# Kernel tuning notes

Hardware: AMD Instinct MI355X
Metric: run time of the kernel (lower is better)

Reference implementation:

```python
import jax, jax.numpy as jnp
import numpy as np

N_NODES, N_EDGES = 100000, 1600000
D_IN, D_H, D_OUT = 256, 128, 32


def _gcn_conv(x, W, b, row, col, norm, n):
    # GCNConv: transform, normalized gather from source nodes, scatter-sum at targets, bias.
    h = x @ W                                   # [n, d_out]
    msgs = h[row] * norm[:, None]               # [E', d_out] edge messages
    out = jax.ops.segment_sum(msgs, col, num_segments=n)
    return out + b


def setup_inputs() -> dict:
    key = jax.random.key(0)
    k = jax.random.split(key, 6)
    x = jax.random.normal(k[0], (N_NODES, D_IN), dtype=jnp.float32)
    edge_index = jax.random.randint(k[1], (2, N_EDGES), 0, N_NODES, dtype=jnp.int64)
    # Glorot-ish scaled params (GCNConv lin has no bias; bias added post-aggregation)
    W1 = jax.random.normal(k[2], (D_IN, D_H), dtype=jnp.float32) * (1.0 / np.sqrt(D_IN))
    b1 = jnp.zeros((D_H,), dtype=jnp.float32)
    W2 = jax.random.normal(k[3], (D_H, D_OUT), dtype=jnp.float32) * (1.0 / np.sqrt(D_H))
    b2 = jnp.zeros((D_OUT,), dtype=jnp.float32)
    return {"x": x, "W1": W1, "b1": b1, "W2": W2, "b2": b2, "edge_index": edge_index}


def reference(x, W1, b1, W2, b2, edge_index):
    n = x.shape[0]
    loops = jnp.arange(n, dtype=edge_index.dtype)
    row = jnp.concatenate([edge_index[0], loops])   # sources (incl. self-loops)
    col = jnp.concatenate([edge_index[1], loops])   # targets
    # symmetric normalization deg^{-1/2} (deg >= 1 because of self-loops)
    deg = jax.ops.segment_sum(jnp.ones_like(col, dtype=x.dtype), col, num_segments=n)
    dinv = deg ** -0.5
    norm = dinv[row] * dinv[col]
    h = jax.nn.relu(_gcn_conv(x, W1, b1, row, col, norm, n))
    # F.dropout(training=False) is identity in eval mode
    out = _gcn_conv(h, W2, b2, row, col, norm, n)
    return jax.nn.log_softmax(out, axis=1)
```

## Files before the change

kernel.cpp:

```cpp
#include <hip/hip_runtime.h>
#include <math.h>

#define N_NODES 100000
#define N_EDGES 1600000
#define D_IN 256
#define D_H 128
#define D_OUT 32
#define N_PAD 102400
#define NB 196
#define CAPB 10240
#define CHUNK 4096

typedef long long ll;
typedef unsigned int uint;
typedef unsigned short ushort;
typedef unsigned char uchar;
typedef short frag_ab __attribute__((ext_vector_type(8)));
typedef float frag_cd __attribute__((ext_vector_type(4)));

__device__ __forceinline__ ushort f2bf(float f) {
    uint u = __float_as_uint(f);
    u += 0x7FFFu + ((u >> 16) & 1u);
    return (ushort)(u >> 16);
}
__device__ __forceinline__ float bfl(uint u) { return __uint_as_float(u << 16); }
__device__ __forceinline__ float bfh(uint u) { return __uint_as_float(u & 0xFFFF0000u); }
__device__ __forceinline__ uint packbf(float a, float b) {
    return (uint)f2bf(a) | ((uint)f2bf(b) << 16);
}

__global__ __launch_bounds__(256) void k_prep(const float* __restrict__ W1,
                                              const float* __restrict__ W2,
                                              ushort* __restrict__ w1t,
                                              ushort* __restrict__ w2t,
                                              int* __restrict__ gcur) {
    int gi = blockIdx.x * 256 + threadIdx.x;
    if (blockIdx.x == 0) gcur[threadIdx.x] = 0;
    if (gi < D_IN * D_H) {
        int k = gi >> 7, nn = gi & 127;
        w1t[nn * D_IN + k] = f2bf(W1[gi]);
    } else if (gi < D_IN * D_H + D_H * D_OUT) {
        int j = gi - D_IN * D_H;
        int k = j >> 5, nn = j & 31;
        w2t[nn * D_H + k] = f2bf(W2[j]);
    }
}

__global__ __launch_bounds__(256, 3) void k_fused(const int* __restrict__ row,
                                                  const int* __restrict__ col,
                                                  int* __restrict__ gcur,
                                                  uint* __restrict__ pairs,
                                                  const float* __restrict__ x,
                                                  const ushort* __restrict__ w1t,
                                                  ushort* __restrict__ hxs,
                                                  int n, int e) {
    __shared__ int cnt[NB];
    __shared__ int lofs[NB];
    __shared__ int lstart[NB];
    __shared__ int sc[256];
    __shared__ uint spair[CHUNK];
    __shared__ uchar sbuck[CHUNK];
    const int t = threadIdx.x;
    const int GA = (e + CHUNK - 1) / CHUNK;
    const int bid = blockIdx.x;

    if (bid < GA) {
        if (t < NB) cnt[t] = 0;
        __syncthreads();
        const int base = bid * CHUNK;
        const int end = min(base + CHUNK, e);
        const int valid = end - base;
        int rs[16], cs[16];
#pragma unroll
        for (int j = 0; j < 16; j++) {
            int idx = base + t + j * 256;
            bool ok = idx < end;
            int c = ok ? col[idx] : 0;
            rs[j] = ok ? row[idx] : 0;
            cs[j] = ok ? c : -1;
            if (ok) atomicAdd(&cnt[c >> 9], 1);
        }
        __syncthreads();
        int v = (t < NB) ? cnt[t] : 0;
        sc[t] = v;
        __syncthreads();
        for (int o = 1; o < 256; o <<= 1) {
            int u2 = (t >= o) ? sc[t - o] : 0;
            __syncthreads();
            sc[t] += u2;
            __syncthreads();
        }
        if (t < NB) {
            lofs[t] = sc[t] - v;
            lstart[t] = (v > 0) ? atomicAdd(&gcur[t], v) : 0;
            cnt[t] = 0;
        }
        __syncthreads();
#pragma unroll
        for (int j = 0; j < 16; j++) {
            int c = cs[j];
            if (c >= 0) {
                int b = c >> 9;
                int pos = lofs[b] + atomicAdd(&cnt[b], 1);
                spair[pos] = ((uint)rs[j] << 9) | (uint)(c & 511);
                sbuck[pos] = (uchar)b;
            }
        }
        __syncthreads();
        for (int i = t; i < valid; i += 256) {
            int b = sbuck[i];
            int rel = lstart[b] + (i - lofs[b]);
            if (rel < CAPB) pairs[b * CAPB + rel] = spair[i];
        }
    } else {
        const int id = bid - GA;
        const int wv = t >> 6, lane = t & 63;
        const int lm = lane & 15, quad = lane >> 4;
        const int base = id * 128 + wv * 32;

        frag_cd acc[2][8];
#pragma unroll
        for (int mt = 0; mt < 2; mt++)
#pragma unroll
            for (int nt = 0; nt < 8; nt++) acc[mt][nt] = (frag_cd){0.f, 0.f, 0.f, 0.f};

        const float4* xr[2];
#pragma unroll
        for (int mt = 0; mt < 2; mt++) {
            int node = base + mt * 16 + lm;
            xr[mt] = (const float4*)(x + (ll)min(node, n - 1) * D_IN);
        }

#pragma unroll
        for (int ks = 0; ks < 8; ks++) {
            frag_ab a[2];
#pragma unroll
            for (int mt = 0; mt < 2; mt++) {
                float4 v0 = xr[mt][ks * 8 + quad * 2];
                float4 v1 = xr[mt][ks * 8 + quad * 2 + 1];
                uint* ap = (uint*)&a[mt];
                ap[0] = packbf(v0.x, v0.y);
                ap[1] = packbf(v0.z, v0.w);
                ap[2] = packbf(v1.x, v1.y);
                ap[3] = packbf(v1.z, v1.w);
            }
#pragma unroll
            for (int nt = 0; nt < 8; nt++) {
                frag_ab b = *(const frag_ab*)&w1t[(nt * 16 + lm) * D_IN + ks * 32 + quad * 8];
#pragma unroll
                for (int mt = 0; mt < 2; mt++)
                    acc[mt][nt] = __builtin_amdgcn_mfma_f32_16x16x32_bf16(
                        a[mt], b, acc[mt][nt], 0, 0, 0);
            }
        }

#pragma unroll
        for (int mt = 0; mt < 2; mt++) {
#pragma unroll
            for (int r = 0; r < 4; r++) {
                int node = base + mt * 16 + quad * 4 + r;
                if (node < n) {
#pragma unroll
                    for (int nt = 0; nt < 8; nt++)
                        hxs[(ll)node * D_H + nt * 16 + lm] = f2bf(acc[mt][nt][r]);
                }
            }
        }
    }
}

__global__ __launch_bounds__(512) void k_fillB(const uint* __restrict__ pairs,
                                               const int* __restrict__ gcur,
                                               int* __restrict__ deg,
                                               int* __restrict__ rp,
                                               float* __restrict__ dinv,
                                               int* __restrict__ csr_src, int n) {
    __shared__ int scsr[CAPB];
    __shared__ int hcnt[512];
    __shared__ int cur[512];
    __shared__ int ssum[512];
    const int b = blockIdx.x, t = threadIdx.x;
    const int node0 = b << 9;
    hcnt[t] = 0;
    __syncthreads();
    const int cnt = min(gcur[b], CAPB);
    const uint* pr = pairs + b * CAPB;
    for (int i = t; i < cnt; i += 512) atomicAdd(&hcnt[pr[i] & 511], 1);
    __syncthreads();
    int d = hcnt[t];
    ssum[t] = d;
    __syncthreads();
    for (int o = 1; o < 512; o <<= 1) {
        int u2 = (t >= o) ? ssum[t - o] : 0;
        __syncthreads();
        ssum[t] += u2;
        __syncthreads();
    }
    int excl = ssum[t] - d;
    cur[t] = excl;
    {
        int vv = node0 + t;
        if (vv < n) {
            rp[vv] = b * CAPB + excl;
            deg[vv] = d;
            dinv[vv] = rsqrtf((float)(1 + d));
        }
    }
    __syncthreads();
    for (int i = t; i < cnt; i += 512) {
        uint pp = pr[i];
        int pos = atomicAdd(&cur[pp & 511], 1);
        if (pos < CAPB) scsr[pos] = (int)(pp >> 9);
    }
    __syncthreads();
    for (int i = t; i < cnt; i += 512)
        csr_src[b * CAPB + i] = scsr[i];
}

__global__ __launch_bounds__(256, 8) void k_agg1f(const uint* __restrict__ hxs,
                                                  const int* __restrict__ csr_src,
                                                  const int* __restrict__ rp,
                                                  const int* __restrict__ deg,
                                                  const float* __restrict__ dinv,
                                                  const float* __restrict__ b1,
                                                  const ushort* __restrict__ w2t,
                                                  ushort* __restrict__ hx2s, int n) {
    __shared__ uint lds_h[16 * 68];
    const int t = threadIdx.x;
    const int w = t >> 6, lane = t & 63;
    const int lm = lane & 15, quad = lane >> 4;
    const int nbase = blockIdx.x * 16;

    float2 bb = ((const float2*)b1)[lane];
#pragma unroll
    for (int q = 0; q < 4; q++) {
        int v = nbase + w * 4 + q;
        float dv = dinv[v];
        uint u = hxs[v * 64 + lane];
        float a0 = dv * bfl(u), a1 = dv * bfh(u);
        int s = rp[v], e = s + deg[v];
        int i = s;
        for (; i + 7 < e; i += 8) {
            int s0 = csr_src[i], s1 = csr_src[i + 1];
            int s2 = csr_src[i + 2], s3 = csr_src[i + 3];
            int s4 = csr_src[i + 4], s5 = csr_src[i + 5];
            int s6 = csr_src[i + 6], s7 = csr_src[i + 7];
            float n0 = dinv[s0], n1 = dinv[s1], n2 = dinv[s2], n3 = dinv[s3];
            float n4 = dinv[s4], n5 = dinv[s5], n6 = dinv[s6], n7 = dinv[s7];
            uint u0 = hxs[s0 * 64 + lane], u1 = hxs[s1 * 64 + lane];
            uint u2 = hxs[s2 * 64 + lane], u3 = hxs[s3 * 64 + lane];
            uint u4 = hxs[s4 * 64 + lane], u5 = hxs[s5 * 64 + lane];
            uint u6 = hxs[s6 * 64 + lane], u7 = hxs[s7 * 64 + lane];
            a0 = fmaf(n0, bfl(u0), a0); a0 = fmaf(n1, bfl(u1), a0);
            a0 = fmaf(n2, bfl(u2), a0); a0 = fmaf(n3, bfl(u3), a0);
            a0 = fmaf(n4, bfl(u4), a0); a0 = fmaf(n5, bfl(u5), a0);
            a0 = fmaf(n6, bfl(u6), a0); a0 = fmaf(n7, bfl(u7), a0);
            a1 = fmaf(n0, bfh(u0), a1); a1 = fmaf(n1, bfh(u1), a1);
            a1 = fmaf(n2, bfh(u2), a1); a1 = fmaf(n3, bfh(u3), a1);
            a1 = fmaf(n4, bfh(u4), a1); a1 = fmaf(n5, bfh(u5), a1);
            a1 = fmaf(n6, bfh(u6), a1); a1 = fmaf(n7, bfh(u7), a1);
        }
        for (; i + 1 < e; i += 2) {
            int s0 = csr_src[i], s1 = csr_src[i + 1];
            float n0 = dinv[s0], n1 = dinv[s1];
            uint u0 = hxs[s0 * 64 + lane], u1 = hxs[s1 * 64 + lane];
            a0 = fmaf(n0, bfl(u0), a0); a0 = fmaf(n1, bfl(u1), a0);
            a1 = fmaf(n0, bfh(u0), a1); a1 = fmaf(n1, bfh(u1), a1);
        }
        if (i < e) {
            int s0 = csr_src[i];
            float n0 = dinv[s0];
            uint u0 = hxs[s0 * 64 + lane];
            a0 = fmaf(n0, bfl(u0), a0);
            a1 = fmaf(n0, bfh(u0), a1);
        }
        lds_h[(w * 4 + q) * 68 + lane] = packbf(fmaxf(fmaf(dv, a0, bb.x), 0.f),
                                                fmaxf(fmaf(dv, a1, bb.y), 0.f));
    }
    __syncthreads();

    if (w < 2) {
        frag_cd acc = (frag_cd){0.f, 0.f, 0.f, 0.f};
#pragma unroll
        for (int c = 0; c < 4; c++) {
            frag_ab a = *(const frag_ab*)&lds_h[lm * 68 + 16 * c + 4 * quad];
            frag_ab b = *(const frag_ab*)&w2t[(w * 16 + lm) * D_H + c * 32 + quad * 8];
            acc = __builtin_amdgcn_mfma_f32_16x16x32_bf16(a, b, acc, 0, 0, 0);
        }
#pragma unroll
        for (int r = 0; r < 4; r++) {
            int node = nbase + quad * 4 + r;
            float dv = dinv[node];
            hx2s[node * D_OUT + w * 16 + lm] = f2bf(acc[r] * dv);
        }
    }
}

__global__ __launch_bounds__(256, 8) void k_agg2(const uint* __restrict__ hx2s,
                                                 const int* __restrict__ csr_src,
                                                 const int* __restrict__ rp,
                                                 const int* __restrict__ deg,
                                                 const float* __restrict__ dinv,
                                                 const float* __restrict__ b2,
                                                 float2* __restrict__ out, int n) {
    int v = blockIdx.x * 16 + (threadIdx.x >> 4);
    if (v >= n) return;
    int l16 = threadIdx.x & 15;
    uint u = hx2s[v * 16 + l16];
    float a0 = bfl(u), a1 = bfh(u);
    int s = rp[v], e = s + deg[v];
    int i = s;
    for (; i + 7 < e; i += 8) {
        int s0 = csr_src[i], s1 = csr_src[i + 1];
        int s2 = csr_src[i + 2], s3 = csr_src[i + 3];
        int s4 = csr_src[i + 4], s5 = csr_src[i + 5];
        int s6 = csr_src[i + 6], s7 = csr_src[i + 7];
        uint u0 = hx2s[s0 * 16 + l16], u1 = hx2s[s1 * 16 + l16];
        uint u2 = hx2s[s2 * 16 + l16], u3 = hx2s[s3 * 16 + l16];
        uint u4 = hx2s[s4 * 16 + l16], u5 = hx2s[s5 * 16 + l16];
        uint u6 = hx2s[s6 * 16 + l16], u7 = hx2s[s7 * 16 + l16];
        a0 += bfl(u0) + bfl(u1) + bfl(u2) + bfl(u3) + bfl(u4) + bfl(u5) + bfl(u6) + bfl(u7);
        a1 += bfh(u0) + bfh(u1) + bfh(u2) + bfh(u3) + bfh(u4) + bfh(u5) + bfh(u6) + bfh(u7);
    }
    for (; i + 1 < e; i += 2) {
        int s0 = csr_src[i], s1 = csr_src[i + 1];
        uint u0 = hx2s[s0 * 16 + l16], u1 = hx2s[s1 * 16 + l16];
        a0 += bfl(u0) + bfl(u1);
        a1 += bfh(u0) + bfh(u1);
    }
    if (i < e) {
        uint u0 = hx2s[csr_src[i] * 16 + l16];
        a0 += bfl(u0);
        a1 += bfh(u0);
    }
    float dv = dinv[v];
    float2 bb = ((const float2*)b2)[l16];
    float t0 = fmaf(dv, a0, bb.x), t1 = fmaf(dv, a1, bb.y);
    float mx = fmaxf(t0, t1);
#pragma unroll
    for (int m = 8; m >= 1; m >>= 1) mx = fmaxf(mx, __shfl_xor(mx, m));
    float sum = __expf(t0 - mx) + __expf(t1 - mx);
#pragma unroll
    for (int m = 8; m >= 1; m >>= 1) sum += __shfl_xor(sum, m);
    float lse = mx + __logf(sum);
    out[v * 16 + l16] = make_float2(t0 - lse, t1 - lse);
}

extern "C" void kernel_launch(void* const* d_in, const int* in_sizes, int n_in,
                              void* d_out, int out_size, void* d_ws, size_t ws_size,
                              hipStream_t stream) {
    const float* x  = (const float*)d_in[0];
    const float* W1 = (const float*)d_in[1];
    const float* b1 = (const float*)d_in[2];
    const float* W2 = (const float*)d_in[3];
    const float* b2 = (const float*)d_in[4];
    const int*   ei = (const int*)d_in[5];
    const int* row = ei;
    const int* col = ei + N_EDGES;

    int*    ws_i    = (int*)d_ws;
    int*    deg     = ws_i;
    int*    gcur    = ws_i + N_PAD;
    int*    rp      = ws_i + N_PAD + 256;
    float*  dinv    = (float*)(ws_i + 2 * N_PAD + 256);
    int*    csr_src = ws_i + 3 * N_PAD + 256;
    uint*   pairs   = (uint*)(csr_src + NB * CAPB);
    ushort* w1t     = (ushort*)(pairs + NB * CAPB);
    ushort* w2t     = w1t + D_IN * D_H;
    ushort* hxs     = w2t + D_H * D_OUT;
    ushort* h_unused= hxs + (ll)N_NODES * D_H;
    ushort* hx2s    = h_unused + (ll)N_NODES * D_H;

    const int n = N_NODES, e = N_EDGES;

    k_prep<<<(D_IN * D_H + D_H * D_OUT + 255) / 256, 256, 0, stream>>>(W1, W2, w1t, w2t, gcur);

    const int GA = (e + CHUNK - 1) / CHUNK;
    const int GG = (n + 127) / 128;
    k_fused<<<GA + GG, 256, 0, stream>>>(row, col, gcur, pairs, x, w1t, hxs, n, e);

    k_fillB<<<NB, 512, 0, stream>>>(pairs, gcur, deg, rp, dinv, csr_src, n);
    k_agg1f<<<n / 16, 256, 0, stream>>>((const uint*)hxs, csr_src, rp, deg, dinv, b1,
                                        w2t, hx2s, n);
    k_agg2<<<(n + 15) / 16, 256, 0, stream>>>((const uint*)hx2s, csr_src, rp, deg, dinv, b2,
                                              (float2*)d_out, n);
}
```

Baseline: 325.8 us.

## Pre-scale GEMM1 output by dinv and drop per-edge dinv gathers in layer-1 aggregation

Splits the fused partition+GEMM kernel into separate partition and GEMM kernels, and moves the GEMM after CSR construction so it can multiply each output row by its source node's dinv. The layer-1 aggregation then sums the pre-scaled rows directly, removing one random dinv gather and one FMA multiply per edge. In exchange, the partition and GEMM no longer overlap in a single launch, and the bf16 rounding now happens after scaling.

```diff
diff --git a/kernel.cpp b/kernel.cpp
--- a/kernel.cpp
+++ b/kernel.cpp
@@ -46,14 +46,10 @@
     }
 }
 
-__global__ __launch_bounds__(256, 3) void k_fused(const int* __restrict__ row,
-                                                  const int* __restrict__ col,
-                                                  int* __restrict__ gcur,
-                                                  uint* __restrict__ pairs,
-                                                  const float* __restrict__ x,
-                                                  const ushort* __restrict__ w1t,
-                                                  ushort* __restrict__ hxs,
-                                                  int n, int e) {
+__global__ __launch_bounds__(256, 3) void k_part(const int* __restrict__ row,
+                                                 const int* __restrict__ col,
+                                                 int* __restrict__ gcur,
+                                                 uint* __restrict__ pairs, int e) {
     __shared__ int cnt[NB];
     __shared__ int lofs[NB];
     __shared__ int lstart[NB];
@@ -61,109 +57,112 @@
     __shared__ uint spair[CHUNK];
     __shared__ uchar sbuck[CHUNK];
     const int t = threadIdx.x;
-    const int GA = (e + CHUNK - 1) / CHUNK;
     const int bid = blockIdx.x;
 
-    if (bid < GA) {
-        if (t < NB) cnt[t] = 0;
+    if (t < NB) cnt[t] = 0;
+    __syncthreads();
+    const int base = bid * CHUNK;
+    const int end = min(base + CHUNK, e);
+    const int valid = end - base;
+    int rs[16], cs[16];
+#pragma unroll
+    for (int j = 0; j < 16; j++) {
+        int idx = base + t + j * 256;
+        bool ok = idx < end;
+        int c = ok ? col[idx] : 0;
+        rs[j] = ok ? row[idx] : 0;
+        cs[j] = ok ? c : -1;
+        if (ok) atomicAdd(&cnt[c >> 9], 1);
+    }
+    __syncthreads();
+    int v = (t < NB) ? cnt[t] : 0;
+    sc[t] = v;
+    __syncthreads();
+    for (int o = 1; o < 256; o <<= 1) {
+        int u2 = (t >= o) ? sc[t - o] : 0;
         __syncthreads();
-        const int base = bid * CHUNK;
-        const int end = min(base + CHUNK, e);
-        const int valid = end - base;
-        int rs[16], cs[16];
-#pragma unroll
-        for (int j = 0; j < 16; j++) {
-            int idx = base + t + j * 256;
-            bool ok = idx < end;
-            int c = ok ? col[idx] : 0;
-            rs[j] = ok ? row[idx] : 0;
-            cs[j] = ok ? c : -1;
-            if (ok) atomicAdd(&cnt[c >> 9], 1);
-        }
+        sc[t] += u2;
         __syncthreads();
-        int v = (t < NB) ? cnt[t] : 0;
-        sc[t] = v;
-        __syncthreads();
-        for (int o = 1; o < 256; o <<= 1) {
-            int u2 = (t >= o) ? sc[t - o] : 0;
-            __syncthreads();
-            sc[t] += u2;
-            __syncthreads();
-        }
-        if (t < NB) {
-            lofs[t] = sc[t] - v;
-            lstart[t] = (v > 0) ? atomicAdd(&gcur[t], v) : 0;
-            cnt[t] = 0;
-        }
-        __syncthreads();
-#pragma unroll
-        for (int j = 0; j < 16; j++) {
-            int c = cs[j];
-            if (c >= 0) {
-                int b = c >> 9;
-                int pos = lofs[b] + atomicAdd(&cnt[b], 1);
-                spair[pos] = ((uint)rs[j] << 9) | (uint)(c & 511);
-                sbuck[pos] = (uchar)b;
-            }
-        }
-        __syncthreads();
-        for (int i = t; i < valid; i += 256) {
-            int b = sbuck[i];
-            int rel = lstart[b] + (i - lofs[b]);
-            if (rel < CAPB) pairs[b * CAPB + rel] = spair[i];
-        }
-    } else {
-        const int id = bid - GA;
-        const int wv = t >> 6, lane = t & 63;
-        const int lm = lane & 15, quad = lane >> 4;
-        const int base = id * 128 + wv * 32;
-
-        frag_cd acc[2][8];
-#pragma unroll
-        for (int mt = 0; mt < 2; mt++)
-#pragma unroll
-            for (int nt = 0; nt < 8; nt++) acc[mt][nt] = (frag_cd){0.f, 0.f, 0.f, 0.f};
-
-        const float4* xr[2];
+    }
+    if (t < NB) {
+        lofs[t] = sc[t] - v;
+        lstart[t] = (v > 0) ? atomicAdd(&gcur[t], v) : 0;
+        cnt[t] = 0;
+    }
+    __syncthreads();
+#pragma unroll
+    for (int j = 0; j < 16; j++) {
+        int c = cs[j];
+        if (c >= 0) {
+            int b = c >> 9;
+            int pos = lofs[b] + atomicAdd(&cnt[b], 1);
+            spair[pos] = ((uint)rs[j] << 9) | (uint)(c & 511);
+            sbuck[pos] = (uchar)b;
+        }
+    }
+    __syncthreads();
+    for (int i = t; i < valid; i += 256) {
+        int b = sbuck[i];
+        int rel = lstart[b] + (i - lofs[b]);
+        if (rel < CAPB) pairs[b * CAPB + rel] = spair[i];
+    }
+}
+
+__global__ __launch_bounds__(256, 3) void k_gemm1(const float* __restrict__ x,
+                                                  const ushort* __restrict__ w1t,
+                                                  const float* __restrict__ dinv,
+                                                  ushort* __restrict__ hxs, int n) {
+    const int t = threadIdx.x;
+    const int wv = t >> 6, lane = t & 63;
+    const int lm = lane & 15, quad = lane >> 4;
+    const int base = blockIdx.x * 128 + wv * 32;
+
+    frag_cd acc[2][8];
+#pragma unroll
+    for (int mt = 0; mt < 2; mt++)
+#pragma unroll
+        for (int nt = 0; nt < 8; nt++) acc[mt][nt] = (frag_cd){0.f, 0.f, 0.f, 0.f};
+
+    const float4* xr[2];
+#pragma unroll
+    for (int mt = 0; mt < 2; mt++) {
+        int node = base + mt * 16 + lm;
+        xr[mt] = (const float4*)(x + (ll)min(node, n - 1) * D_IN);
+    }
+
+#pragma unroll
+    for (int ks = 0; ks < 8; ks++) {
+        frag_ab a[2];
 #pragma unroll
         for (int mt = 0; mt < 2; mt++) {
-            int node = base + mt * 16 + lm;
-            xr[mt] = (const float4*)(x + (ll)min(node, n - 1) * D_IN);
-        }
-
-#pragma unroll
-        for (int ks = 0; ks < 8; ks++) {
-            frag_ab a[2];
-#pragma unroll
-            for (int mt = 0; mt < 2; mt++) {
-                float4 v0 = xr[mt][ks * 8 + quad * 2];
-                float4 v1 = xr[mt][ks * 8 + quad * 2 + 1];
-                uint* ap = (uint*)&a[mt];
-                ap[0] = packbf(v0.x, v0.y);
-                ap[1] = packbf(v0.z, v0.w);
-                ap[2] = packbf(v1.x, v1.y);
-                ap[3] = packbf(v1.z, v1.w);
-            }
-#pragma unroll
-            for (int nt = 0; nt < 8; nt++) {
-                frag_ab b = *(const frag_ab*)&w1t[(nt * 16 + lm) * D_IN + ks * 32 + quad * 8];
-#pragma unroll
-                for (int mt = 0; mt < 2; mt++)
-                    acc[mt][nt] = __builtin_amdgcn_mfma_f32_16x16x32_bf16(
-                        a[mt], b, acc[mt][nt], 0, 0, 0);
-            }
-        }
-
-#pragma unroll
-        for (int mt = 0; mt < 2; mt++) {
-#pragma unroll
-            for (int r = 0; r < 4; r++) {
-                int node = base + mt * 16 + quad * 4 + r;
-                if (node < n) {
-#pragma unroll
-                    for (int nt = 0; nt < 8; nt++)
-                        hxs[(ll)node * D_H + nt * 16 + lm] = f2bf(acc[mt][nt][r]);
-                }
+            float4 v0 = xr[mt][ks * 8 + quad * 2];
+            float4 v1 = xr[mt][ks * 8 + quad * 2 + 1];
+            uint* ap = (uint*)&a[mt];
+            ap[0] = packbf(v0.x, v0.y);
+            ap[1] = packbf(v0.z, v0.w);
+            ap[2] = packbf(v1.x, v1.y);
+            ap[3] = packbf(v1.z, v1.w);
+        }
+#pragma unroll
+        for (int nt = 0; nt < 8; nt++) {
+            frag_ab b = *(const frag_ab*)&w1t[(nt * 16 + lm) * D_IN + ks * 32 + quad * 8];
+#pragma unroll
+            for (int mt = 0; mt < 2; mt++)
+                acc[mt][nt] = __builtin_amdgcn_mfma_f32_16x16x32_bf16(
+                    a[mt], b, acc[mt][nt], 0, 0, 0);
+        }
+    }
+
+#pragma unroll
+    for (int mt = 0; mt < 2; mt++) {
+#pragma unroll
+        for (int r = 0; r < 4; r++) {
+            int node = base + mt * 16 + quad * 4 + r;
+            if (node < n) {
+                float dv = dinv[node];
+#pragma unroll
+                for (int nt = 0; nt < 8; nt++)
+                    hxs[(ll)node * D_H + nt * 16 + lm] = f2bf(acc[mt][nt][r] * dv);
             }
         }
     }
@@ -237,7 +236,7 @@
         int v = nbase + w * 4 + q;
         float dv = dinv[v];
         uint u = hxs[v * 64 + lane];
-        float a0 = dv * bfl(u), a1 = dv * bfh(u);
+        float a0 = bfl(u), a1 = bfh(u);
         int s = rp[v], e = s + deg[v];
         int i = s;
         for (; i + 7 < e; i += 8) {
@@ -245,34 +244,23 @@
             int s2 = csr_src[i + 2], s3 = csr_src[i + 3];
             int s4 = csr_src[i + 4], s5 = csr_src[i + 5];
             int s6 = csr_src[i + 6], s7 = csr_src[i + 7];
-            float n0 = dinv[s0], n1 = dinv[s1], n2 = dinv[s2], n3 = dinv[s3];
-            float n4 = dinv[s4], n5 = dinv[s5], n6 = dinv[s6], n7 = dinv[s7];
             uint u0 = hxs[s0 * 64 + lane], u1 = hxs[s1 * 64 + lane];
             uint u2 = hxs[s2 * 64 + lane], u3 = hxs[s3 * 64 + lane];
             uint u4 = hxs[s4 * 64 + lane], u5 = hxs[s5 * 64 + lane];
             uint u6 = hxs[s6 * 64 + lane], u7 = hxs[s7 * 64 + lane];
-            a0 = fmaf(n0, bfl(u0), a0); a0 = fmaf(n1, bfl(u1), a0);
-            a0 = fmaf(n2, bfl(u2), a0); a0 = fmaf(n3, bfl(u3), a0);
-            a0 = fmaf(n4, bfl(u4), a0); a0 = fmaf(n5, bfl(u5), a0);
-            a0 = fmaf(n6, bfl(u6), a0); a0 = fmaf(n7, bfl(u7), a0);
-            a1 = fmaf(n0, bfh(u0), a1); a1 = fmaf(n1, bfh(u1), a1);
-            a1 = fmaf(n2, bfh(u2), a1); a1 = fmaf(n3, bfh(u3), a1);
-            a1 = fmaf(n4, bfh(u4), a1); a1 = fmaf(n5, bfh(u5), a1);
-            a1 = fmaf(n6, bfh(u6), a1); a1 = fmaf(n7, bfh(u7), a1);
+            a0 += bfl(u0) + bfl(u1) + bfl(u2) + bfl(u3) + bfl(u4) + bfl(u5) + bfl(u6) + bfl(u7);
+            a1 += bfh(u0) + bfh(u1) + bfh(u2) + bfh(u3) + bfh(u4) + bfh(u5) + bfh(u6) + bfh(u7);
         }
         for (; i + 1 < e; i += 2) {
             int s0 = csr_src[i], s1 = csr_src[i + 1];
-            float n0 = dinv[s0], n1 = dinv[s1];
             uint u0 = hxs[s0 * 64 + lane], u1 = hxs[s1 * 64 + lane];
-            a0 = fmaf(n0, bfl(u0), a0); a0 = fmaf(n1, bfl(u1), a0);
-            a1 = fmaf(n0, bfh(u0), a1); a1 = fmaf(n1, bfh(u1), a1);
+            a0 += bfl(u0) + bfl(u1);
+            a1 += bfh(u0) + bfh(u1);
         }
         if (i < e) {
-            int s0 = csr_src[i];
-            float n0 = dinv[s0];
-            uint u0 = hxs[s0 * 64 + lane];
-            a0 = fmaf(n0, bfl(u0), a0);
-            a1 = fmaf(n0, bfh(u0), a1);
+            uint u0 = hxs[csr_src[i] * 64 + lane];
+            a0 += bfl(u0);
+            a1 += bfh(u0);
         }
         lds_h[(w * 4 + q) * 68 + lane] = packbf(fmaxf(fmaf(dv, a0, bb.x), 0.f),
                                                 fmaxf(fmaf(dv, a1, bb.y), 0.f));
@@ -368,18 +356,17 @@
     ushort* w1t     = (ushort*)(pairs + NB * CAPB);
     ushort* w2t     = w1t + D_IN * D_H;
     ushort* hxs     = w2t + D_H * D_OUT;
-    ushort* h_unused= hxs + (ll)N_NODES * D_H;
-    ushort* hx2s    = h_unused + (ll)N_NODES * D_H;
+    ushort* spare   = hxs + (ll)N_NODES * D_H;
+    ushort* hx2s    = spare + (ll)N_NODES * D_H;
 
     const int n = N_NODES, e = N_EDGES;
 
     k_prep<<<(D_IN * D_H + D_H * D_OUT + 255) / 256, 256, 0, stream>>>(W1, W2, w1t, w2t, gcur);
 
     const int GA = (e + CHUNK - 1) / CHUNK;
-    const int GG = (n + 127) / 128;
-    k_fused<<<GA + GG, 256, 0, stream>>>(row, col, gcur, pairs, x, w1t, hxs, n, e);
-
+    k_part<<<GA, 256, 0, stream>>>(row, col, gcur, pairs, e);
     k_fillB<<<NB, 512, 0, stream>>>(pairs, gcur, deg, rp, dinv, csr_src, n);
+    k_gemm1<<<(n + 127) / 128, 256, 0, stream>>>(x, w1t, dinv, hxs, n);
     k_agg1f<<<n / 16, 256, 0, stream>>>((const uint*)hxs, csr_src, rp, deg, dinv, b1,
                                         w2t, hx2s, n);
     k_agg2<<<(n + 15) / 16, 256, 0, stream>>>((const uint*)hx2s, csr_src, rp, deg, dinv, b2,
```

Measured after the change: 323.8 us. Within noise of the previous version (-0.6%).

## Regroup stage fusion: partition with weight prep, CSR fill with GEMM

Applied to the files above, without the earlier changes.

The weight transpose/convert kernel is merged into the edge-partition kernel, and the CSR fill is merged with the first dense GEMM, so the GEMM now overlaps the bucket-to-CSR step instead of the partition step. The gcur reset moves to a hipMemsetAsync. The GEMM blocks now use 512 threads, each covering 256 nodes. The aim is to drop one launch and balance the fused grids, at the cost of the GEMM running under the fillB kernel's launch bounds and large LDS footprint, which may lower its occupancy.

```diff
diff --git a/kernel.cpp b/kernel.cpp
--- a/kernel.cpp
+++ b/kernel.cpp
@@ -10,6 +10,7 @@
 #define NB 196
 #define CAPB 10240
 #define CHUNK 4096
+#define NW (D_IN * D_H + D_H * D_OUT)
 
 typedef long long ll;
 typedef unsigned int uint;
@@ -29,31 +30,14 @@
     return (uint)f2bf(a) | ((uint)f2bf(b) << 16);
 }
 
-__global__ __launch_bounds__(256) void k_prep(const float* __restrict__ W1,
-                                              const float* __restrict__ W2,
-                                              ushort* __restrict__ w1t,
-                                              ushort* __restrict__ w2t,
-                                              int* __restrict__ gcur) {
-    int gi = blockIdx.x * 256 + threadIdx.x;
-    if (blockIdx.x == 0) gcur[threadIdx.x] = 0;
-    if (gi < D_IN * D_H) {
-        int k = gi >> 7, nn = gi & 127;
-        w1t[nn * D_IN + k] = f2bf(W1[gi]);
-    } else if (gi < D_IN * D_H + D_H * D_OUT) {
-        int j = gi - D_IN * D_H;
-        int k = j >> 5, nn = j & 31;
-        w2t[nn * D_H + k] = f2bf(W2[j]);
-    }
-}
-
-__global__ __launch_bounds__(256, 3) void k_fused(const int* __restrict__ row,
-                                                  const int* __restrict__ col,
-                                                  int* __restrict__ gcur,
-                                                  uint* __restrict__ pairs,
-                                                  const float* __restrict__ x,
-                                                  const ushort* __restrict__ w1t,
-                                                  ushort* __restrict__ hxs,
-                                                  int n, int e) {
+__global__ __launch_bounds__(256, 3) void k_part(const int* __restrict__ row,
+                                                 const int* __restrict__ col,
+                                                 int* __restrict__ gcur,
+                                                 uint* __restrict__ pairs,
+                                                 const float* __restrict__ W1,
+                                                 const float* __restrict__ W2,
+                                                 ushort* __restrict__ w1t,
+                                                 ushort* __restrict__ w2t, int e) {
     __shared__ int cnt[NB];
     __shared__ int lofs[NB];
     __shared__ int lstart[NB];
@@ -64,59 +48,126 @@
     const int GA = (e + CHUNK - 1) / CHUNK;
     const int bid = blockIdx.x;
 
-    if (bid < GA) {
-        if (t < NB) cnt[t] = 0;
-        __syncthreads();
-        const int base = bid * CHUNK;
-        const int end = min(base + CHUNK, e);
-        const int valid = end - base;
-        int rs[16], cs[16];
-#pragma unroll
-        for (int j = 0; j < 16; j++) {
-            int idx = base + t + j * 256;
-            bool ok = idx < end;
-            int c = ok ? col[idx] : 0;
-            rs[j] = ok ? row[idx] : 0;
-            cs[j] = ok ? c : -1;
-            if (ok) atomicAdd(&cnt[c >> 9], 1);
-        }
-        __syncthreads();
-        int v = (t < NB) ? cnt[t] : 0;
-        sc[t] = v;
-        __syncthreads();
-        for (int o = 1; o < 256; o <<= 1) {
-            int u2 = (t >= o) ? sc[t - o] : 0;
+    if (bid >= GA) {
+        int gi = (bid - GA) * 256 + t;
+        if (gi < D_IN * D_H) {
+            int k = gi >> 7, nn = gi & 127;
+            w1t[nn * D_IN + k] = f2bf(W1[gi]);
+        } else if (gi < NW) {
+            int j = gi - D_IN * D_H;
+            int k = j >> 5, nn = j & 31;
+            w2t[nn * D_H + k] = f2bf(W2[j]);
+        }
+        return;
+    }
+
+    if (t < NB) cnt[t] = 0;
+    __syncthreads();
+    const int base = bid * CHUNK;
+    const int end = min(base + CHUNK, e);
+    const int valid = end - base;
+    int rs[16], cs[16];
+#pragma unroll
+    for (int j = 0; j < 16; j++) {
+        int idx = base + t + j * 256;
+        bool ok = idx < end;
+        int c = ok ? col[idx] : 0;
+        rs[j] = ok ? row[idx] : 0;
+        cs[j] = ok ? c : -1;
+        if (ok) atomicAdd(&cnt[c >> 9], 1);
+    }
+    __syncthreads();
+    int v = (t < NB) ? cnt[t] : 0;
+    sc[t] = v;
+    __syncthreads();
+    for (int o = 1; o < 256; o <<= 1) {
+        int u2 = (t >= o) ? sc[t - o] : 0;
+        __syncthreads();
+        sc[t] += u2;
+        __syncthreads();
+    }
+    if (t < NB) {
+        lofs[t] = sc[t] - v;
+        lstart[t] = (v > 0) ? atomicAdd(&gcur[t], v) : 0;
+        cnt[t] = 0;
+    }
+    __syncthreads();
+#pragma unroll
+    for (int j = 0; j < 16; j++) {
+        int c = cs[j];
+        if (c >= 0) {
+            int b = c >> 9;
+            int pos = lofs[b] + atomicAdd(&cnt[b], 1);
+            spair[pos] = ((uint)rs[j] << 9) | (uint)(c & 511);
+            sbuck[pos] = (uchar)b;
+        }
+    }
+    __syncthreads();
+    for (int i = t; i < valid; i += 256) {
+        int b = sbuck[i];
+        int rel = lstart[b] + (i - lofs[b]);
+        if (rel < CAPB) pairs[b * CAPB + rel] = spair[i];
+    }
+}
+
+__global__ __launch_bounds__(512) void k_fused2(const uint* __restrict__ pairs,
+                                                const int* __restrict__ gcur,
+                                                int* __restrict__ deg,
+                                                int* __restrict__ rp,
+                                                float* __restrict__ dinv,
+                                                int* __restrict__ csr_src,
+                                                const float* __restrict__ x,
+                                                const ushort* __restrict__ w1t,
+                                                ushort* __restrict__ hxs, int n) {
+    __shared__ int scsr[CAPB];
+    __shared__ int hcnt[512];
+    __shared__ int cur[512];
+    __shared__ int ssum[512];
+    const int t = threadIdx.x;
+    const int bid = blockIdx.x;
+
+    if (bid < NB) {
+        const int b = bid;
+        const int node0 = b << 9;
+        hcnt[t] = 0;
+        __syncthreads();
+        const int cnt = min(gcur[b], CAPB);
+        const uint* pr = pairs + b * CAPB;
+        for (int i = t; i < cnt; i += 512) atomicAdd(&hcnt[pr[i] & 511], 1);
+        __syncthreads();
+        int d = hcnt[t];
+        ssum[t] = d;
+        __syncthreads();
+        for (int o = 1; o < 512; o <<= 1) {
+            int u2 = (t >= o) ? ssum[t - o] : 0;
             __syncthreads();
-            sc[t] += u2;
+            ssum[t] += u2;
             __syncthreads();
         }
-        if (t < NB) {
-            lofs[t] = sc[t] - v;
-            lstart[t] = (v > 0) ? atomicAdd(&gcur[t], v) : 0;
-            cnt[t] = 0;
-        }
-        __syncthreads();
-#pragma unroll
-        for (int j = 0; j < 16; j++) {
-            int c = cs[j];
-            if (c >= 0) {
-                int b = c >> 9;
-                int pos = lofs[b] + atomicAdd(&cnt[b], 1);
-                spair[pos] = ((uint)rs[j] << 9) | (uint)(c & 511);
-                sbuck[pos] = (uchar)b;
+        int excl = ssum[t] - d;
+        cur[t] = excl;
+        {
+            int vv = node0 + t;
+            if (vv < n) {
+                rp[vv] = b * CAPB + excl;
+                deg[vv] = d;
+                dinv[vv] = rsqrtf((float)(1 + d));
             }
         }
         __syncthreads();
-        for (int i = t; i < valid; i += 256) {
-            int b = sbuck[i];
-            int rel = lstart[b] + (i - lofs[b]);
-            if (rel < CAPB) pairs[b * CAPB + rel] = spair[i];
-        }
+        for (int i = t; i < cnt; i += 512) {
+            uint pp = pr[i];
+            int pos = atomicAdd(&cur[pp & 511], 1);
+            if (pos < CAPB) scsr[pos] = (int)(pp >> 9);
+        }
+        __syncthreads();
+        for (int i = t; i < cnt; i += 512)
+            csr_src[b * CAPB + i] = scsr[i];
     } else {
-        const int id = bid - GA;
+        const int id = bid - NB;
         const int wv = t >> 6, lane = t & 63;
         const int lm = lane & 15, quad = lane >> 4;
-        const int base = id * 128 + wv * 32;
+        const int base = id * 256 + wv * 32;
 
         frag_cd acc[2][8];
 #pragma unroll
@@ -167,54 +218,6 @@
             }
         }
     }
-}
-
-__global__ __launch_bounds__(512) void k_fillB(const uint* __restrict__ pairs,
-                                               const int* __restrict__ gcur,
-                                               int* __restrict__ deg,
-                                               int* __restrict__ rp,
-                                               float* __restrict__ dinv,
-                                               int* __restrict__ csr_src, int n) {
-    __shared__ int scsr[CAPB];
-    __shared__ int hcnt[512];
-    __shared__ int cur[512];
-    __shared__ int ssum[512];
-    const int b = blockIdx.x, t = threadIdx.x;
-    const int node0 = b << 9;
-    hcnt[t] = 0;
-    __syncthreads();
-    const int cnt = min(gcur[b], CAPB);
-    const uint* pr = pairs + b * CAPB;
-    for (int i = t; i < cnt; i += 512) atomicAdd(&hcnt[pr[i] & 511], 1);
-    __syncthreads();
-    int d = hcnt[t];
-    ssum[t] = d;
-    __syncthreads();
-    for (int o = 1; o < 512; o <<= 1) {
-        int u2 = (t >= o) ? ssum[t - o] : 0;
-        __syncthreads();
-        ssum[t] += u2;
-        __syncthreads();
-    }
-    int excl = ssum[t] - d;
-    cur[t] = excl;
-    {
-        int vv = node0 + t;
-        if (vv < n) {
-            rp[vv] = b * CAPB + excl;
-            deg[vv] = d;
-            dinv[vv] = rsqrtf((float)(1 + d));
-        }
-    }
-    __syncthreads();
-    for (int i = t; i < cnt; i += 512) {
-        uint pp = pr[i];
-        int pos = atomicAdd(&cur[pp & 511], 1);
-        if (pos < CAPB) scsr[pos] = (int)(pp >> 9);
-    }
-    __syncthreads();
-    for (int i = t; i < cnt; i += 512)
-        csr_src[b * CAPB + i] = scsr[i];
 }
 
 __global__ __launch_bounds__(256, 8) void k_agg1f(const uint* __restrict__ hxs,
@@ -368,18 +371,20 @@
     ushort* w1t     = (ushort*)(pairs + NB * CAPB);
     ushort* w2t     = w1t + D_IN * D_H;
     ushort* hxs     = w2t + D_H * D_OUT;
-    ushort* h_unused= hxs + (ll)N_NODES * D_H;
-    ushort* hx2s    = h_unused + (ll)N_NODES * D_H;
+    ushort* spare   = hxs + (ll)N_NODES * D_H;
+    ushort* hx2s    = spare + (ll)N_NODES * D_H;
 
     const int n = N_NODES, e = N_EDGES;
 
-    k_prep<<<(D_IN * D_H + D_H * D_OUT + 255) / 256, 256, 0, stream>>>(W1, W2, w1t, w2t, gcur);
+    hipMemsetAsync(gcur, 0, 256 * sizeof(int), stream);
 
     const int GA = (e + CHUNK - 1) / CHUNK;
-    const int GG = (n + 127) / 128;
-    k_fused<<<GA + GG, 256, 0, stream>>>(row, col, gcur, pairs, x, w1t, hxs, n, e);
-
-    k_fillB<<<NB, 512, 0, stream>>>(pairs, gcur, deg, rp, dinv, csr_src, n);
+    k_part<<<GA + NW / 256, 256, 0, stream>>>(row, col, gcur, pairs, W1, W2, w1t, w2t, e);
+
+    const int GG = (n + 255) / 256;
+    k_fused2<<<NB + GG, 512, 0, stream>>>(pairs, gcur, deg, rp, dinv, csr_src,
+                                          x, w1t, hxs, n);
+
     k_agg1f<<<n / 16, 256, 0, stream>>>((const uint*)hxs, csr_src, rp, deg, dinv, b1,
                                         w2t, hx2s, n);
     k_agg2<<<(n + 15) / 16, 256, 0, stream>>>((const uint*)hx2s, csr_src, rp, deg, dinv, b2,
```

After: 325.1 us. Within noise of the previous version (-0.2%).
